# Kernel tuning notes

Hardware: AMD Instinct MI355X
Metric: run time of the kernel (lower is better)

Reference implementation:

```python
import jax, jax.numpy as jnp
import numpy as np

PARTS = [list(range(0, 17)), list(range(17, 22)), list(range(22, 27)),
         list(range(27, 36)), list(range(36, 42)), list(range(42, 48)),
         list(range(48, 68))]
NUM_PARTS = len(PARTS)
V_JOINTS = max(max(p) for p in PARTS) + 1  # 68
# joint -> part index (same as get_corr_joints)
JOINTS = np.zeros((V_JOINTS,), dtype=np.int32)
for j, part in enumerate(PARTS):
    for i in part:
        JOINTS[i] = j
BN_EPS = 1e-5


def setup_inputs() -> dict:
    key = jax.random.key(0)
    k0, k1, k2 = jax.random.split(key, 3)
    N, C, T, V = 512, 1024, 1, V_JOINTS
    x = jax.random.normal(k0, (N, C, T, V), dtype=jnp.float32)
    conv1_w = jax.random.normal(k1, (C // 4, C), dtype=jnp.float32) * 0.02  # 1x1 conv C->C/4
    conv1_b = jnp.zeros((C // 4,), dtype=jnp.float32)
    conv2_w = jax.random.normal(k2, (2,), dtype=jnp.float32) * 0.5  # 1x1 conv 2->1
    conv2_b = jnp.zeros((), dtype=jnp.float32)
    bn_gamma = jnp.ones((C,), dtype=jnp.float32)
    bn_beta = jnp.zeros((C,), dtype=jnp.float32)
    return {"x": x, "conv1_w": conv1_w, "conv1_b": conv1_b,
            "conv2_w": conv2_w, "conv2_b": conv2_b,
            "bn_gamma": bn_gamma, "bn_beta": bn_beta}


def _forward(x, conv1_w, conv1_b, conv2_w, conv2_b, bn_gamma, bn_beta):
    N, C, T, V = x.shape  # T must be 1 (required by original .view)
    joints = jnp.asarray(JOINTS)
    P = NUM_PARTS
    # part-wise mean pool over joints: (V,P) normalized one-hot
    M = jax.nn.one_hot(joints, P, dtype=x.dtype)
    M = M / jnp.sum(M, axis=0, keepdims=True)
    x_parts = jnp.einsum('nctv,vp->nctp', x, M)            # (N,C,T,P)
    # conv1: 1x1, C -> C/4
    h = jnp.einsum('nctp,oc->notp', x_parts, conv1_w) + conv1_b[None, :, None, None]
    x_cap = jnp.mean(h, axis=1, keepdims=True)             # channel avg pool
    x_cmp = jnp.max(h, axis=1, keepdims=True)              # channel max pool
    # conv2: 1x1, 2 -> 1 (cat order is (avg, max))
    att = conv2_w[0] * x_cap + conv2_w[1] * x_cmp + conv2_b  # (N,1,T,P)
    att = jnp.broadcast_to(att, (N, C, T, P)).reshape(N, C, P)
    att = jax.nn.softmax(att, axis=-1)                     # softmax over parts
    # scatter part attention back to joints
    att_j = att[:, :, joints][:, :, None, :]               # (N,C,1,V)
    y = x * att_j
    # BatchNorm2d (training mode: batch stats over N,T,V per channel)
    mean = jnp.mean(y, axis=(0, 2, 3), keepdims=True)
    var = jnp.var(y, axis=(0, 2, 3), keepdims=True)
    y_bn = (y - mean) * jax.lax.rsqrt(var + BN_EPS)
    y_bn = y_bn * bn_gamma[None, :, None, None] + bn_beta[None, :, None, None]
    return jax.nn.relu(y_bn + x)


def reference(x, conv1_w, conv1_b, conv2_w, conv2_b, bn_gamma, bn_beta):
    return _forward(x, conv1_w, conv1_b, conv2_w, conv2_b, bn_gamma, bn_beta)
```

## Files before the change

kernel.cpp:

```cpp
#include <hip/hip_runtime.h>

#define NN 512
#define CC 1024
#define OO 256
#define VV 68
#define PP 7
#define NC (NN*CC)
#define NV_CNT 34816.0f

typedef float floatx4 __attribute__((ext_vector_type(4)));

__device__ __forceinline__ int part_of(int v){
  return (v>=17)+(v>=22)+(v>=27)+(v>=36)+(v>=42)+(v>=48);
}

__global__ __launch_bounds__(256) void k0_prep(const float* __restrict__ w1,
    float* __restrict__ w1p){
  int g = blockIdx.x*256 + threadIdx.x;
  int o = g >> 8, cb = g & 255;
  float4 v = ((const float4*)w1)[g];
  ((float4*)w1p)[cb*256 + o] = v;
}

__global__ __launch_bounds__(256) void k1_partsum(const float* __restrict__ x,
    float* __restrict__ S, float* __restrict__ S2){
  __shared__ float stg[68*129];
  int R = blockIdx.x*128;
  const float4* src = (const float4*)(x + (size_t)R*VV);
  #pragma unroll
  for (int k=0;k<9;k++){
    int g = k*256 + threadIdx.x;
    if (k==8 && threadIdx.x>=128) break;
    float4 v4 = src[g];
    int row = g/17, q = g - row*17;
    stg[(q*4+0)*129 + row] = v4.x;
    stg[(q*4+1)*129 + row] = v4.y;
    stg[(q*4+2)*129 + row] = v4.z;
    stg[(q*4+3)*129 + row] = v4.w;
  }
  __syncthreads();

  int row  = threadIdx.x & 127;
  int half = threadIdx.x >> 7;
  float s[PP], q2[PP];
  #pragma unroll
  for (int p=0;p<PP;p++){ s[p]=0.f; q2[p]=0.f; }
  int v0 = half*34;
  #pragma unroll
  for (int i=0;i<34;i++){
    int v = v0 + i;
    int p = part_of(v);
    float e = stg[v*129 + row];
    s[p] += e;
    q2[p] = fmaf(e, e, q2[p]);
  }
  __syncthreads();
  float* hs = stg;
  float* hq = stg + 128*PP;
  if (half==1){
    #pragma unroll
    for (int p=0;p<PP;p++){ hs[row*PP+p]=s[p]; hq[row*PP+p]=q2[p]; }
  }
  __syncthreads();
  if (half==0){
    int r = R + row;
    #pragma unroll
    for (int p=0;p<PP;p++){
      S [p*NC + r] = s[p]  + hs[row*PP+p];
      S2[p*NC + r] = q2[p] + hq[row*PP+p];
    }
  }
}

__global__ __launch_bounds__(256) void k2_att(const float* __restrict__ S,
    const float* __restrict__ S2, const float* __restrict__ w1p,
    const float* __restrict__ b1, const float* __restrict__ w2,
    const float* __restrict__ b2, float* __restrict__ att,
    float* __restrict__ partial){
  int n = blockIdx.x;
  int t = threadIdx.x;

  __shared__ float4 sSf4[PP*256];
  __shared__ float hred[2048];
  __shared__ float red_s[4][PP], red_m[4][PP], pre[PP], att_s[PP];
  float* sSl = (float*)sSf4;

  for (int u = t; u < PP*256; u += 256){
    int p = u >> 8, cb = u & 255;
    sSf4[u] = *(const float4*)(S + (size_t)p*NC + (size_t)n*CC + cb*4);
  }
  __syncthreads();

  int oh = t & 31, ch = t >> 5;
  float acc[8][PP];
  #pragma unroll
  for (int k=0;k<8;k++)
    #pragma unroll
    for (int p=0;p<PP;p++) acc[k][p] = 0.f;

  const float4* wp = (const float4*)w1p;
  for (int i=0;i<32;i++){
    int gcb = ch*32 + i;
    const float4* wrow = wp + (size_t)gcb*256 + oh;
    float4 w[8];
    #pragma unroll
    for (int k=0;k<8;k++) w[k] = wrow[32*k];
    #pragma unroll
    for (int p=0;p<PP;p++){
      float4 sv = sSf4[p*256 + gcb];
      #pragma unroll
      for (int k=0;k<8;k++){
        acc[k][p] = fmaf(w[k].x, sv.x, acc[k][p]);
        acc[k][p] = fmaf(w[k].y, sv.y, acc[k][p]);
        acc[k][p] = fmaf(w[k].z, sv.z, acc[k][p]);
        acc[k][p] = fmaf(w[k].w, sv.w, acc[k][p]);
      }
    }
  }

  const float inv_cnt[PP] = {1.f/17.f,1.f/5.f,1.f/5.f,1.f/9.f,1.f/6.f,1.f/6.f,1.f/20.f};
  float bo = b1[t];
  float h[PP];
  #pragma unroll
  for (int p=0;p<PP;p++){
    __syncthreads();
    #pragma unroll
    for (int k=0;k<8;k++) hred[ch*256 + k*32 + oh] = acc[k][p];
    __syncthreads();
    float hs = 0.f;
    #pragma unroll
    for (int c8=0;c8<8;c8++) hs += hred[c8*256 + t];
    h[p] = fmaf(hs, inv_cnt[p], bo);
  }

  int lane = t & 63, wid = t >> 6;
  #pragma unroll
  for (int p=0;p<PP;p++){
    float sm = h[p], mx = h[p];
    #pragma unroll
    for (int off=32; off>0; off>>=1){
      sm += __shfl_down(sm, off, 64);
      mx = fmaxf(mx, __shfl_down(mx, off, 64));
    }
    if (lane==0){ red_s[wid][p]=sm; red_m[wid][p]=mx; }
  }
  __syncthreads();
  if (t < PP){
    int p = t;
    float sm = red_s[0][p]+red_s[1][p]+red_s[2][p]+red_s[3][p];
    float mx = fmaxf(fmaxf(red_m[0][p],red_m[1][p]),
                     fmaxf(red_m[2][p],red_m[3][p]));
    pre[p] = w2[0]*(sm*(1.f/(float)OO)) + w2[1]*mx + b2[0];
  }
  __syncthreads();
  if (t == 0){
    float m = pre[0];
    #pragma unroll
    for (int p=1;p<PP;p++) m = fmaxf(m, pre[p]);
    float e[PP], sum=0.f;
    #pragma unroll
    for (int p=0;p<PP;p++){ e[p] = expf(pre[p]-m); sum += e[p]; }
    float inv = 1.f/sum;
    #pragma unroll
    for (int p=0;p<PP;p++){
      float a = e[p]*inv;
      att_s[p] = a;
      att[n*PP+p] = a;
    }
  }
  __syncthreads();

  float a[PP], a2[PP];
  #pragma unroll
  for (int p=0;p<PP;p++){ a[p] = att_s[p]; a2[p] = a[p]*a[p]; }
  const float* S2n = S2 + (size_t)n*CC;
  #pragma unroll
  for (int j=0;j<4;j++){
    int c = j*256 + t;
    float sm=0.f, sq=0.f;
    #pragma unroll
    for (int p=0;p<PP;p++){
      sm = fmaf(a[p],  sSl[p*1024 + c],   sm);
      sq = fmaf(a2[p], S2n[(size_t)p*NC + c], sq);
    }
    partial[n*2048 + c]        = sm;
    partial[n*2048 + 1024 + c] = sq;
  }
}

__global__ __launch_bounds__(256) void k3b_finalize(const float* __restrict__ partial,
    const float* __restrict__ gamma, const float* __restrict__ beta,
    float* __restrict__ scsh){
  __shared__ float rs[8][32], rq[8][32];
  int cl = threadIdx.x & 31, grp = threadIdx.x >> 5;
  int c = blockIdx.x*32 + cl;
  float sm=0.f, sq=0.f;
  for (int i=0;i<64;i++){
    int n = grp*64 + i;
    sm += partial[n*2048 + c];
    sq += partial[n*2048 + 1024 + c];
  }
  rs[grp][cl] = sm; rq[grp][cl] = sq;
  __syncthreads();
  if (threadIdx.x < 32){
    float tsm=0.f, tsq=0.f;
    #pragma unroll
    for (int g=0; g<8; g++){ tsm += rs[g][threadIdx.x]; tsq += rq[g][threadIdx.x]; }
    int cc = blockIdx.x*32 + threadIdx.x;
    float mean = tsm * (1.0f/NV_CNT);
    float var  = tsq * (1.0f/NV_CNT) - mean*mean;
    float rstd = rsqrtf(var + 1e-5f);
    float sc = gamma[cc]*rstd;
    scsh[cc]        = sc;
    scsh[1024 + cc] = beta[cc] - mean*sc;
  }
}

__global__ __launch_bounds__(256) void k4_out(const float* __restrict__ x,
    const float* __restrict__ att, const float* __restrict__ scsh,
    float* __restrict__ out){
  int f = blockIdx.x*256 + threadIdx.x;
  int n = blockIdx.x / 68;
  __shared__ float s_att[PP];
  if (threadIdx.x < PP) s_att[threadIdx.x] = att[n*PP + threadIdx.x];
  __syncthreads();
  int r = f/17;
  int q = f - r*17;
  int v0 = q*4;
  int c = r & (CC-1);
  float4 xv = ((const float4*)x)[f];
  float sc = scsh[c];
  float sh = scsh[1024 + c];
  float vals[4];
  #pragma unroll
  for (int j=0;j<4;j++){
    int p = part_of(v0 + j);
    float a = s_att[p];
    float e = (j==0)?xv.x:(j==1)?xv.y:(j==2)?xv.z:xv.w;
    vals[j] = fmaxf(fmaf(e, fmaf(a, sc, 1.0f), sh), 0.0f);
  }
  floatx4 ov; ov.x=vals[0]; ov.y=vals[1]; ov.z=vals[2]; ov.w=vals[3];
  __builtin_nontemporal_store(ov, ((floatx4*)out) + f);
}

extern "C" void kernel_launch(void* const* d_in, const int* in_sizes, int n_in,
                              void* d_out, int out_size, void* d_ws, size_t ws_size,
                              hipStream_t stream) {
  const float* x     = (const float*)d_in[0];
  const float* w1    = (const float*)d_in[1];
  const float* b1    = (const float*)d_in[2];
  const float* w2    = (const float*)d_in[3];
  const float* b2    = (const float*)d_in[4];
  const float* gamma = (const float*)d_in[5];
  const float* beta  = (const float*)d_in[6];
  float* out = (float*)d_out;

  float* w1p     = (float*)d_ws;
  float* S       = w1p + OO*CC;
  float* S2      = S + 7*NC;
  float* partial = S2 + 7*NC;
  float* scsh    = partial + NN*2048;
  float* att     = scsh + 2048;

  k0_prep     <<<256,         256, 0, stream>>>(w1, w1p);
  k1_partsum  <<<NC/128,      256, 0, stream>>>(x, S, S2);
  k2_att      <<<NN,          256, 0, stream>>>(S, S2, w1p, b1, w2, b2, att, partial);
  k3b_finalize<<<32,          256, 0, stream>>>(partial, gamma, beta, scsh);
  k4_out      <<<(NC*17)/256, 256, 0, stream>>>(x, att, scsh, out);
}
```

Before: 328.9 us.

## Fuse part-sum pooling into the attention kernel, dropping the S/S2 buffers

The separate part-sum kernel is removed. Each attention block now reads its own sample's rows of x directly: every thread loads one 68-wide row as 17 float4s and computes per-part sums and sums of squares. Sums go to shared memory, while the squared sums stay in registers for the BN partial statistics. This removes the write and re-read of the large S/S2 intermediates in global memory, plus one kernel launch. In exchange, the whole x read now runs in only 512 blocks with heavy register use and strided per-thread row loads, which may reduce memory-level parallelism.

```diff
diff --git a/kernel.cpp b/kernel.cpp
--- a/kernel.cpp
+++ b/kernel.cpp
@@ -22,61 +22,10 @@
   ((float4*)w1p)[cb*256 + o] = v;
 }
 
-__global__ __launch_bounds__(256) void k1_partsum(const float* __restrict__ x,
-    float* __restrict__ S, float* __restrict__ S2){
-  __shared__ float stg[68*129];
-  int R = blockIdx.x*128;
-  const float4* src = (const float4*)(x + (size_t)R*VV);
-  #pragma unroll
-  for (int k=0;k<9;k++){
-    int g = k*256 + threadIdx.x;
-    if (k==8 && threadIdx.x>=128) break;
-    float4 v4 = src[g];
-    int row = g/17, q = g - row*17;
-    stg[(q*4+0)*129 + row] = v4.x;
-    stg[(q*4+1)*129 + row] = v4.y;
-    stg[(q*4+2)*129 + row] = v4.z;
-    stg[(q*4+3)*129 + row] = v4.w;
-  }
-  __syncthreads();
-
-  int row  = threadIdx.x & 127;
-  int half = threadIdx.x >> 7;
-  float s[PP], q2[PP];
-  #pragma unroll
-  for (int p=0;p<PP;p++){ s[p]=0.f; q2[p]=0.f; }
-  int v0 = half*34;
-  #pragma unroll
-  for (int i=0;i<34;i++){
-    int v = v0 + i;
-    int p = part_of(v);
-    float e = stg[v*129 + row];
-    s[p] += e;
-    q2[p] = fmaf(e, e, q2[p]);
-  }
-  __syncthreads();
-  float* hs = stg;
-  float* hq = stg + 128*PP;
-  if (half==1){
-    #pragma unroll
-    for (int p=0;p<PP;p++){ hs[row*PP+p]=s[p]; hq[row*PP+p]=q2[p]; }
-  }
-  __syncthreads();
-  if (half==0){
-    int r = R + row;
-    #pragma unroll
-    for (int p=0;p<PP;p++){
-      S [p*NC + r] = s[p]  + hs[row*PP+p];
-      S2[p*NC + r] = q2[p] + hq[row*PP+p];
-    }
-  }
-}
-
-__global__ __launch_bounds__(256) void k2_att(const float* __restrict__ S,
-    const float* __restrict__ S2, const float* __restrict__ w1p,
-    const float* __restrict__ b1, const float* __restrict__ w2,
-    const float* __restrict__ b2, float* __restrict__ att,
-    float* __restrict__ partial){
+__global__ __launch_bounds__(256) void k12_att(const float* __restrict__ x,
+    const float* __restrict__ w1p, const float* __restrict__ b1,
+    const float* __restrict__ w2, const float* __restrict__ b2,
+    float* __restrict__ att, float* __restrict__ partial){
   int n = blockIdx.x;
   int t = threadIdx.x;
 
@@ -85,9 +34,35 @@
   __shared__ float red_s[4][PP], red_m[4][PP], pre[PP], att_s[PP];
   float* sSl = (float*)sSf4;
 
-  for (int u = t; u < PP*256; u += 256){
-    int p = u >> 8, cb = u & 255;
-    sSf4[u] = *(const float4*)(S + (size_t)p*NC + (size_t)n*CC + cb*4);
+  float q2r[4][PP];
+
+  const float4* xb = (const float4*)(x + (size_t)n*CC*VV);
+  #pragma unroll
+  for (int j=0;j<4;j++){
+    int r = j*256 + t;
+    const float4* rp = xb + (size_t)r*17;
+    float4 d[17];
+    #pragma unroll
+    for (int k=0;k<17;k++) d[k] = rp[k];
+    float s[PP], q2[PP];
+    #pragma unroll
+    for (int p=0;p<PP;p++){ s[p]=0.f; q2[p]=0.f; }
+    #pragma unroll
+    for (int k=0;k<17;k++){
+      #pragma unroll
+      for (int c4=0;c4<4;c4++){
+        int v = 4*k + c4;
+        int p = part_of(v);
+        float e = (c4==0)?d[k].x:(c4==1)?d[k].y:(c4==2)?d[k].z:d[k].w;
+        s[p] += e;
+        q2[p] = fmaf(e, e, q2[p]);
+      }
+    }
+    #pragma unroll
+    for (int p=0;p<PP;p++){
+      sSl[p*1024 + r] = s[p];
+      q2r[j][p] = q2[p];
+    }
   }
   __syncthreads();
 
@@ -173,15 +148,14 @@
   float a[PP], a2[PP];
   #pragma unroll
   for (int p=0;p<PP;p++){ a[p] = att_s[p]; a2[p] = a[p]*a[p]; }
-  const float* S2n = S2 + (size_t)n*CC;
   #pragma unroll
   for (int j=0;j<4;j++){
     int c = j*256 + t;
-    float sm=0.f, sq=0.f;
-    #pragma unroll
-    for (int p=0;p<PP;p++){
-      sm = fmaf(a[p],  sSl[p*1024 + c],   sm);
-      sq = fmaf(a2[p], S2n[(size_t)p*NC + c], sq);
+    float sm = 0.f, sq = 0.f;
+    #pragma unroll
+    for (int p=0;p<PP;p++){
+      sm = fmaf(a[p],  sSl[p*1024 + c], sm);
+      sq = fmaf(a2[p], q2r[j][p],       sq);
     }
     partial[n*2048 + c]        = sm;
     partial[n*2048 + 1024 + c] = sq;
@@ -256,15 +230,12 @@
   float* out = (float*)d_out;
 
   float* w1p     = (float*)d_ws;
-  float* S       = w1p + OO*CC;
-  float* S2      = S + 7*NC;
-  float* partial = S2 + 7*NC;
+  float* partial = w1p + OO*CC;
   float* scsh    = partial + NN*2048;
   float* att     = scsh + 2048;
 
   k0_prep     <<<256,         256, 0, stream>>>(w1, w1p);
-  k1_partsum  <<<NC/128,      256, 0, stream>>>(x, S, S2);
-  k2_att      <<<NN,          256, 0, stream>>>(S, S2, w1p, b1, w2, b2, att, partial);
+  k12_att     <<<NN,          256, 0, stream>>>(x, w1p, b1, w2, b2, att, partial);
   k3b_finalize<<<32,          256, 0, stream>>>(partial, gamma, beta, scsh);
   k4_out      <<<(NC*17)/256, 256, 0, stream>>>(x, att, scsh, out);
 }
```

Measured after the change: 356.0 us. 8.2% more time.
